# Kernel optimization log

Hardware: AMD Instinct MI355X
Metric: run time of the kernel (lower is better)

Reference implementation:

```python
import jax, jax.numpy as jnp
import numpy as np

N_STATE = 4      # d_state from CrossMambaFusionBlock(d_state=4)
DT_RANK = 48     # ceil(768/16), standard Mamba dt_rank='auto'
D_CONV = 4       # depthwise causal conv kernel size


def _ln(x, g, b):
    m = jnp.mean(x, axis=-1, keepdims=True)
    v = jnp.mean((x - m) ** 2, axis=-1, keepdims=True)
    return (x - m) * jax.lax.rsqrt(v + 1e-5) * g + b


def _dwconv1d(u, w, b):
    # u: (B,L,D); w: (D,1,K) depthwise causal conv along token dim L
    K = w.shape[-1]
    up = jnp.pad(jnp.transpose(u, (0, 2, 1)), ((0, 0), (0, 0), (K - 1, 0)))
    out = jax.lax.conv_general_dilated(up, w, (1,), 'VALID',
                                       feature_group_count=w.shape[0],
                                       dimension_numbers=('NCH', 'OIH', 'NCH'))
    return jnp.transpose(out, (0, 2, 1)) + b


def _pre(x, g, b, Win, Wconv, bconv, Wxp, Wdt, bdt):
    # LayerNorm -> in_proj -> depthwise conv + SiLU -> dt/B/C projections
    B_, H, W, C = x.shape
    xn = _ln(x, g, b).reshape(B_, H * W, C)
    u, z = jnp.split(xn @ Win, 2, axis=-1)              # (B,L,D) each
    u = jax.nn.silu(_dwconv1d(u, Wconv, bconv))
    dbl = u @ Wxp                                        # (B,L,R+2N)
    dtr, Bm, Cm = jnp.split(dbl, [DT_RANK, DT_RANK + N_STATE], axis=-1)
    dt = jax.nn.softplus(dtr @ Wdt + bdt)                # (B,L,D)
    return u, z, dt, Bm, Cm


def _selective_scan(u, dt, Alog, Bm, Cm, Dskip):
    # u, dt: (B,L,D); Alog: (D,N); Bm, Cm: (B,L,N)
    A = -jnp.exp(Alog)
    dA = jnp.exp(dt[..., None] * A)                      # (B,L,D,N) decay
    dBu = (dt * u)[..., None] * Bm[:, :, None, :]        # (B,L,D,N) input

    def comb(c1, c2):
        a1, h1 = c1
        a2, h2 = c2
        return a1 * a2, a2 * h1 + h2

    _, h = jax.lax.associative_scan(comb, (dA, dBu), axis=1)
    return jnp.einsum('bldn,bln->bld', h, Cm) + u * Dskip


def _forward(x1, x2,
             ln_g1, ln_b1, Win1, Wconv1, bconv1, Wxp1, Wdt1, bdt1, Alog1, Dskip1, Wout1,
             ln_g2, ln_b2, Win2, Wconv2, bconv2, Wxp2, Wdt2, bdt2, Alog2, Dskip2, Wout2):
    x1 = jnp.transpose(x1, (0, 2, 3, 1))  # BCHW -> BHWC (as in forward_features)
    x2 = jnp.transpose(x2, (0, 2, 3, 1))
    B_, H, W, C = x1.shape
    u1, z1, dt1, B1, C1 = _pre(x1, ln_g1, ln_b1, Win1, Wconv1, bconv1, Wxp1, Wdt1, bdt1)
    u2, z2, dt2, B2, C2 = _pre(x2, ln_g2, ln_b2, Win2, Wconv2, bconv2, Wxp2, Wdt2, bdt2)
    # Cross-modal fusion: each stream's SSM state is read out with the OTHER
    # stream's C projection (cross selective scan).
    y1 = _selective_scan(u1, dt1, Alog1, B1, C2, Dskip1)
    y2 = _selective_scan(u2, dt2, Alog2, B2, C1, Dskip2)
    o1 = ((y1 * jax.nn.silu(z1)) @ Wout1).reshape(B_, H, W, C)
    o2 = ((y2 * jax.nn.silu(z2)) @ Wout2).reshape(B_, H, W, C)
    return x1 + o1, x2 + o2


def setup_inputs():
    key = jax.random.key(0)
    ks = jax.random.split(key, 16)
    B_, C, H, W = 2, 768, 64, 64
    D = C  # d_inner (ssm_ratio = 1)

    def nrm(k, shape, s=0.02):
        return jax.random.normal(k, shape, jnp.float32) * s

    inp = {
        'x1': jax.random.normal(ks[0], (B_, C, H, W), jnp.float32),
        'x2': jax.random.normal(ks[1], (B_, C, H, W), jnp.float32),
    }
    for i, o in ((1, 2), (2, 8)):
        inp[f'ln_g{i}'] = jnp.ones((C,), jnp.float32)
        inp[f'ln_b{i}'] = jnp.zeros((C,), jnp.float32)
        inp[f'Win{i}'] = nrm(ks[o], (C, 2 * D))
        inp[f'Wconv{i}'] = nrm(ks[o + 1], (D, 1, D_CONV), 0.1)
        inp[f'bconv{i}'] = jnp.zeros((D,), jnp.float32)
        inp[f'Wxp{i}'] = nrm(ks[o + 2], (D, DT_RANK + 2 * N_STATE))
        inp[f'Wdt{i}'] = nrm(ks[o + 3], (DT_RANK, D), 0.05)
        inp[f'bdt{i}'] = jnp.full((D,), -4.6, jnp.float32)  # softplus -> dt ~ 0.01
        inp[f'Alog{i}'] = jnp.log(jnp.broadcast_to(
            jnp.arange(1, N_STATE + 1, dtype=jnp.float32), (D, N_STATE)))
        inp[f'Dskip{i}'] = jnp.ones((D,), jnp.float32)
        inp[f'Wout{i}'] = nrm(ks[o + 4], (D, C))
    return inp


def reference(x1, x2,
              ln_g1, ln_b1, Win1, Wconv1, bconv1, Wxp1, Wdt1, bdt1, Alog1, Dskip1, Wout1,
              ln_g2, ln_b2, Win2, Wconv2, bconv2, Wxp2, Wdt2, bdt2, Alog2, Dskip2, Wout2):
    return _forward(x1, x2,
                    ln_g1, ln_b1, Win1, Wconv1, bconv1, Wxp1, Wdt1, bdt1, Alog1, Dskip1, Wout1,
                    ln_g2, ln_b2, Win2, Wconv2, bconv2, Wxp2, Wdt2, bdt2, Alog2, Dskip2, Wout2)
```

## Files before the change

### kernel.cpp

```cpp
#include <hip/hip_runtime.h>
#include <cmath>

#define LDIM 4096
#define CDIM 768
#define BDIM 2
#define NST 4
#define RNK 48
#define CH 64
#define LC 64
#define NDT 896

typedef short bf16x8 __attribute__((ext_vector_type(8)));
typedef float f32x4 __attribute__((ext_vector_type(4)));

__device__ __forceinline__ float sigmoidf_(float x) { return 1.f / (1.f + __expf(-x)); }

__device__ __forceinline__ unsigned short f2bf(float f) {
    unsigned int u = __float_as_uint(f);
    u += 0x7fffu + ((u >> 16) & 1u);
    return (unsigned short)(u >> 16);
}
__device__ __forceinline__ float bf2f(unsigned short us) {
    unsigned int u = ((unsigned int)us) << 16;
    return __uint_as_float(u);
}

__device__ __forceinline__ void llds16(const unsigned short* g, unsigned short* l) {
    __builtin_amdgcn_global_load_lds(
        (const __attribute__((address_space(1))) unsigned int*)g,
        (__attribute__((address_space(3))) unsigned int*)l, 16, 0, 0);
}

__global__ __launch_bounds__(256) void stats_kernel(const float* __restrict__ x0,
                                                    const float* __restrict__ x1,
                                                    float* __restrict__ stats)
{
    int blk = blockIdx.x;
    int s = blk >> 7;
    int b = (blk >> 6) & 1;
    int l0 = (blk & 63) * 64;
    int wave = threadIdx.x >> 6, lane = threadIdx.x & 63;
    const float* x = s ? x1 : x0;
    const float* xp = x + ((size_t)b * CDIM) * LDIM + l0 + lane;
    float sm = 0.f, sq = 0.f;
    int cbeg = wave * 192;
#pragma unroll
    for (int i0 = 0; i0 < 192; i0 += 16) {
        float v[16];
#pragma unroll
        for (int j = 0; j < 16; j++) v[j] = xp[(size_t)(cbeg + i0 + j) * LDIM];
#pragma unroll
        for (int j = 0; j < 16; j++) { sm += v[j]; sq += v[j] * v[j]; }
    }
    __shared__ float red[2][4][64];
    red[0][wave][lane] = sm;
    red[1][wave][lane] = sq;
    __syncthreads();
    if (wave == 0) {
        float s_ = red[0][0][lane] + red[0][1][lane] + red[0][2][lane] + red[0][3][lane];
        float q_ = red[1][0][lane] + red[1][1][lane] + red[1][2][lane] + red[1][3][lane];
        float m = s_ * (1.f / CDIM);
        float var = q_ * (1.f / CDIM) - m * m;
        int idx = s * 8192 + b * LDIM + l0 + lane;
        stats[2 * idx] = m;
        stats[2 * idx + 1] = rsqrtf(var + 1e-5f);
    }
}

__global__ __launch_bounds__(256) void transpose_ln_kernel(
    const float* __restrict__ x0, const float* __restrict__ x1,
    const float* __restrict__ g0, const float* __restrict__ bb0,
    const float* __restrict__ g1, const float* __restrict__ bb1,
    const float* __restrict__ stats,
    unsigned short* __restrict__ xnb0, unsigned short* __restrict__ xnb1,
    float* __restrict__ out)
{
    __shared__ float tile[64][65];
    int t = threadIdx.x;
    int c0 = blockIdx.x * 64, l0 = blockIdx.y * 64;
    int z = blockIdx.z;
    int s = z >> 1, b = z & 1;
    const float* x = s ? x1 : x0;
    const float* g = s ? g1 : g0;
    const float* bb = s ? bb1 : bb0;
    unsigned short* xnb = s ? xnb1 : xnb0;
    int tl = t & 63, tg = t >> 6;
#pragma unroll
    for (int i = 0; i < 16; i++) {
        int cl = tg * 16 + i;
        tile[cl][tl] = x[((size_t)(b * CDIM + c0 + cl)) * LDIM + l0 + tl];
    }
    __syncthreads();
    const size_t SZ = (size_t)BDIM * LDIM * CDIM;
#pragma unroll
    for (int i = 0; i < 16; i++) {
        int ll = tg * 16 + i;
        int l = l0 + ll, c = c0 + tl;
        float v = tile[tl][ll];
        int sidx = s * 8192 + b * LDIM + l;
        float m = stats[sidx * 2], rs = stats[sidx * 2 + 1];
        size_t o = ((size_t)(b * LDIM + l)) * CDIM + c;
        out[(size_t)s * SZ + o] = v;
        xnb[o] = f2bf((v - m) * rs * g[c] + bb[c]);
    }
}

__global__ __launch_bounds__(256) void wt_transpose_all(
    const float* __restrict__ Win0, const float* __restrict__ Win1,
    const float* __restrict__ Wout0, const float* __restrict__ Wout1,
    unsigned short* __restrict__ WinT0, unsigned short* __restrict__ WinT1,
    unsigned short* __restrict__ WoutT0, unsigned short* __restrict__ WoutT1)
{
    int z = blockIdx.z;
    const float* W = (z == 0) ? Win0 : (z == 1) ? Win1 : (z == 2) ? Wout0 : Wout1;
    unsigned short* Wt = (z == 0) ? WinT0 : (z == 1) ? WinT1 : (z == 2) ? WoutT0 : WoutT1;
    const int K = CDIM;
    const int N = (z < 2) ? 2 * CDIM : CDIM;
    if (blockIdx.x * 64 >= N) return;
    __shared__ float tile[64][65];
    int t = threadIdx.x;
    int n0 = blockIdx.x * 64, k0 = blockIdx.y * 64;
    int tn = t & 63, tg = t >> 6;
#pragma unroll
    for (int i = 0; i < 16; i++) {
        int kl = tg * 16 + i;
        tile[kl][tn] = W[(size_t)(k0 + kl) * N + n0 + tn];
    }
    __syncthreads();
#pragma unroll
    for (int i = 0; i < 16; i++) {
        int nl = tg * 16 + i;
        int k = k0 + tn, n = n0 + nl;
        Wt[(size_t)n * K + k] = f2bf(tile[tn][nl]);
    }
}

__global__ __launch_bounds__(256) void wcomb_kernel(
    const float* __restrict__ Wxp0, const float* __restrict__ Wdt0,
    const float* __restrict__ Wxp1, const float* __restrict__ Wdt1,
    unsigned short* __restrict__ W0, unsigned short* __restrict__ W1)
{
    int s = blockIdx.z;
    const float* Wxp = s ? Wxp1 : Wxp0;
    const float* Wdt = s ? Wdt1 : Wdt0;
    unsigned short* WcombT = s ? W1 : W0;
    int t = threadIdx.x;
    int k = blockIdx.x * 64 + (t & 63);
    int n0 = blockIdx.y * 64;
    float wx[RNK];
#pragma unroll
    for (int r = 0; r < RNK; r++) wx[r] = Wxp[k * 56 + r];
    for (int i = (t >> 6); i < 64; i += 4) {
        int n = n0 + i;
        float val;
        if (n < CDIM) {
            float acc = 0.f;
#pragma unroll
            for (int r = 0; r < RNK; r++) acc += wx[r] * Wdt[(size_t)r * CDIM + n];
            val = acc;
        } else if (n < CDIM + 8) {
            val = Wxp[k * 56 + RNK + (n - CDIM)];
        } else {
            val = 0.f;
        }
        WcombT[(size_t)n * CDIM + k] = f2bf(val);
    }
}

__global__ __launch_bounds__(512, 4) void gemm_mfma(
    const unsigned short* __restrict__ A0, const unsigned short* __restrict__ A1,
    const unsigned short* __restrict__ Bt0, const unsigned short* __restrict__ Bt1,
    void* __restrict__ C0, void* __restrict__ C1, int ldc, int K, int epi,
    const float* __restrict__ bias0, const float* __restrict__ bias1,
    float* __restrict__ D0, float* __restrict__ D1)
{
    const unsigned short* A = blockIdx.z ? A1 : A0;
    const unsigned short* Bt = blockIdx.z ? Bt1 : Bt0;
    void* C = blockIdx.z ? C1 : C0;
    const float* bias = blockIdx.z ? bias1 : bias0;
    float* D = blockIdx.z ? D1 : D0;

    __shared__ unsigned short As[3][128 * 32];
    __shared__ unsigned short Bs[3][128 * 32];
    const int tid = threadIdx.x;
    const int wave = tid >> 6, lane = tid & 63;
    const int row0 = blockIdx.x * 128, col0 = blockIdx.y * 128;
    const int wm = (wave >> 2) * 64, wn = (wave & 3) * 32;
    f32x4 acc[4][2] = {};
    const int lr = lane >> 2;
    const int gi = ((lane & 3) ^ ((lane >> 3) & 3)) * 8;
    const int fr = lane & 15, fc = lane >> 4;

    const unsigned short* ga0 = A + (size_t)(row0 + wave * 16 + lr) * K + gi;
    const unsigned short* gb0 = Bt + (size_t)(col0 + wave * 16 + lr) * K + gi;
    const int rb = wave * 16;

#define ISSUE(st, kb)                         \
    do {                                      \
        llds16(ga0 + (kb), &As[st][rb * 32]); \
        llds16(gb0 + (kb), &Bs[st][rb * 32]); \
    } while (0)

    const int NIT = K / 32;
    ISSUE(0, 0);
    ISSUE(1, 32);
    for (int i = 0; i < NIT; i++) {
        if (i < NIT - 1) __builtin_amdgcn_s_waitcnt(0xF72);
        else __builtin_amdgcn_s_waitcnt(0xF70);
        __builtin_amdgcn_s_barrier();
        if (i + 2 < NIT) ISSUE((i + 2) % 3, (i + 2) * 32);
        const unsigned short* as = As[i % 3];
        const unsigned short* bs = Bs[i % 3];
        bf16x8 af[4], bfr[2];
#pragma unroll
        for (int ii = 0; ii < 4; ii++) {
            int r = wm + ii * 16 + fr;
            af[ii] = *(const bf16x8*)&as[r * 32 + (fc ^ ((r >> 1) & 3)) * 8];
        }
#pragma unroll
        for (int j = 0; j < 2; j++) {
            int r = wn + j * 16 + fr;
            bfr[j] = *(const bf16x8*)&bs[r * 32 + (fc ^ ((r >> 1) & 3)) * 8];
        }
#pragma unroll
        for (int ii = 0; ii < 4; ii++)
#pragma unroll
            for (int j = 0; j < 2; j++)
                acc[ii][j] = __builtin_amdgcn_mfma_f32_16x16x32_bf16(af[ii], bfr[j], acc[ii][j], 0, 0, 0);
    }
#undef ISSUE

    const int cr = (lane >> 4) * 4, cc = lane & 15;
#pragma unroll
    for (int ii = 0; ii < 4; ii++)
#pragma unroll
        for (int j = 0; j < 2; j++) {
            int col = col0 + wn + j * 16 + cc;
#pragma unroll
            for (int r = 0; r < 4; r++) {
                int row = row0 + wm + ii * 16 + cr + r;
                float v = acc[ii][j][r];
                if (epi == 1) {
                    float* Cf = (float*)C;
                    size_t o = (size_t)row * ldc + col;
                    Cf[o] = v + Cf[o];
                } else if (epi == 2) {
                    if (col < CDIM) {
                        v += bias[col];
                        v = (v > 20.f) ? v : __logf(1.f + __expf(v));
                        ((unsigned short*)C)[(size_t)row * ldc + col] = f2bf(v);
                    } else if (col < CDIM + 8) {
                        D[(size_t)row * 8 + (col - CDIM)] = v;
                    }
                } else {
                    ((unsigned short*)C)[(size_t)row * ldc + col] = f2bf(v);
                }
            }
        }
}

__global__ __launch_bounds__(256) void conv_silu_kernel(
    const unsigned short* __restrict__ uzb0, const unsigned short* __restrict__ uzb1,
    const float* __restrict__ w0, const float* __restrict__ bc0,
    const float* __restrict__ w1, const float* __restrict__ bc1,
    unsigned short* __restrict__ ub0, unsigned short* __restrict__ ub1)
{
    int s = blockIdx.y;
    const unsigned short* uzb = s ? uzb1 : uzb0;
    const float* w = s ? w1 : w0;
    const float* bc = s ? bc1 : bc0;
    unsigned short* ub = s ? ub1 : ub0;
    int idx = blockIdx.x * 256 + threadIdx.x;
    int d8 = (idx % 96) * 8;
    int bl = idx / 96;
    int l = bl & (LDIM - 1);

    float wr[8][4];
#pragma unroll
    for (int q = 0; q < 8; q++) {
        f32x4 wv = *(const f32x4*)&w[(d8 + q) * 4];
#pragma unroll
        for (int k = 0; k < 4; k++) wr[q][k] = wv[k];
    }
    float acc[8];
    f32x4 b0 = *(const f32x4*)&bc[d8];
    f32x4 b1 = *(const f32x4*)&bc[d8 + 4];
#pragma unroll
    for (int q = 0; q < 4; q++) { acc[q] = b0[q]; acc[4 + q] = b1[q]; }

#pragma unroll
    for (int k = 0; k < 4; k++) {
        int ls = l - 3 + k;
        if (ls >= 0) {
            bf16x8 uv = *(const bf16x8*)&uzb[(size_t)(bl - 3 + k) * (2 * CDIM) + d8];
#pragma unroll
            for (int q = 0; q < 8; q++)
                acc[q] += bf2f((unsigned short)uv[q]) * wr[q][k];
        }
    }
    bf16x8 ov;
#pragma unroll
    for (int q = 0; q < 8; q++) {
        float v = acc[q];
        ov[q] = (short)f2bf(v * sigmoidf_(v));
    }
    *(bf16x8*)&ub[(size_t)bl * CDIM + d8] = ov;
}

__global__ __launch_bounds__(256) void scan_phaseA(
    const unsigned short* __restrict__ u0, const unsigned short* __restrict__ dt0,
    const float* __restrict__ dbl0, const float* __restrict__ Alog0,
    const unsigned short* __restrict__ u1, const unsigned short* __restrict__ dt1,
    const float* __restrict__ dbl1, const float* __restrict__ Alog1,
    float* __restrict__ agg)
{
    int idx = blockIdx.x * 256 + threadIdx.x;
    int d = idx % CDIM;
    int t1 = idx / CDIM;
    int c = t1 % CH;
    int t2 = t1 / CH;
    int b = t2 & 1;
    int s = t2 >> 1;
    const unsigned short* u = s ? u1 : u0;
    const unsigned short* dt = s ? dt1 : dt0;
    const float* dbl = s ? dbl1 : dbl0;
    const float* Alog = s ? Alog1 : Alog0;
    float A[4];
#pragma unroll
    for (int n = 0; n < 4; n++) A[n] = -__expf(Alog[d * 4 + n]);
    float h[4] = {0, 0, 0, 0}, aa[4] = {1, 1, 1, 1};
    int rowb = b * LDIM + c * LC;
    for (int t = 0; t < LC; t++) {
        int row = rowb + t;
        float dtv = bf2f(dt[(size_t)row * CDIM + d]);
        float uv = bf2f(u[(size_t)row * CDIM + d]);
        float du = dtv * uv;
        const float* bm = dbl + (size_t)row * 8;
#pragma unroll
        for (int n = 0; n < 4; n++) {
            float dA = __expf(dtv * A[n]);
            h[n] = dA * h[n] + du * bm[n];
            aa[n] *= dA;
        }
    }
    float* o = agg + (size_t)idx * 8;
#pragma unroll
    for (int n = 0; n < 4; n++) { o[n] = aa[n]; o[4 + n] = h[n]; }
}

__global__ __launch_bounds__(256) void scan_phaseB(const float* __restrict__ agg,
                                                   float* __restrict__ hinit)
{
    int idx = blockIdx.x * 256 + threadIdx.x;
    int d = idx % CDIM;
    int sb = idx / CDIM;
    float st[4] = {0, 0, 0, 0};
    for (int c = 0; c < CH; c++) {
        size_t base = ((size_t)sb * CH + c) * CDIM + d;
        const float* a = agg + base * 8;
        float* hi = hinit + base * 4;
#pragma unroll
        for (int n = 0; n < 4; n++) hi[n] = st[n];
#pragma unroll
        for (int n = 0; n < 4; n++) st[n] = a[n] * st[n] + a[4 + n];
    }
}

__global__ __launch_bounds__(256) void scan_phaseC(
    const unsigned short* __restrict__ u0, const unsigned short* __restrict__ dt0,
    const unsigned short* __restrict__ uzb0, const float* __restrict__ dbl0,
    const float* __restrict__ Alog0, const float* __restrict__ Dsk0, unsigned short* __restrict__ g0,
    const unsigned short* __restrict__ u1, const unsigned short* __restrict__ dt1,
    const unsigned short* __restrict__ uzb1, const float* __restrict__ dbl1,
    const float* __restrict__ Alog1, const float* __restrict__ Dsk1, unsigned short* __restrict__ g1,
    const float* __restrict__ hinit)
{
    int idx = blockIdx.x * 256 + threadIdx.x;
    int d = idx % CDIM;
    int t1 = idx / CDIM;
    int c = t1 % CH;
    int t2 = t1 / CH;
    int b = t2 & 1;
    int s = t2 >> 1;
    const unsigned short* u = s ? u1 : u0;
    const unsigned short* dt = s ? dt1 : dt0;
    const unsigned short* uzb = s ? uzb1 : uzb0;
    const float* dbl = s ? dbl1 : dbl0;
    const float* dblO = s ? dbl0 : dbl1;
    const float* Alog = s ? Alog1 : Alog0;
    const float* Dsk = s ? Dsk1 : Dsk0;
    unsigned short* gated = s ? g1 : g0;
    float A[4];
#pragma unroll
    for (int n = 0; n < 4; n++) A[n] = -__expf(Alog[d * 4 + n]);
    float Dv = Dsk[d];
    float h[4];
    const float* hi = hinit + (size_t)idx * 4;
#pragma unroll
    for (int n = 0; n < 4; n++) h[n] = hi[n];
    int rowb = b * LDIM + c * LC;
    for (int t = 0; t < LC; t++) {
        int row = rowb + t;
        float dtv = bf2f(dt[(size_t)row * CDIM + d]);
        float uv = bf2f(u[(size_t)row * CDIM + d]);
        float du = dtv * uv;
        const float* bm = dbl + (size_t)row * 8;
        const float* cm = dblO + (size_t)row * 8 + 4;
        float y = 0.f;
#pragma unroll
        for (int n = 0; n < 4; n++) {
            float dA = __expf(dtv * A[n]);
            h[n] = dA * h[n] + du * bm[n];
            y += h[n] * cm[n];
        }
        y += uv * Dv;
        float zv = bf2f(uzb[(size_t)row * (2 * CDIM) + CDIM + d]);
        gated[(size_t)row * CDIM + d] = f2bf(y * (zv * sigmoidf_(zv)));
    }
}

extern "C" void kernel_launch(void* const* d_in, const int* in_sizes, int n_in,
                              void* d_out, int out_size, void* d_ws, size_t ws_size,
                              hipStream_t stream)
{
    const float* x[2] = {(const float*)d_in[0], (const float*)d_in[1]};
    const float *ln_g[2], *ln_b[2], *Win[2], *Wconv[2], *bconv[2], *Wxp[2],
        *Wdt[2], *bdt[2], *Alog[2], *Dskip[2], *Wout[2];
    for (int s = 0; s < 2; s++) {
        int base = 2 + s * 11;
        ln_g[s] = (const float*)d_in[base + 0];
        ln_b[s] = (const float*)d_in[base + 1];
        Win[s] = (const float*)d_in[base + 2];
        Wconv[s] = (const float*)d_in[base + 3];
        bconv[s] = (const float*)d_in[base + 4];
        Wxp[s] = (const float*)d_in[base + 5];
        Wdt[s] = (const float*)d_in[base + 6];
        bdt[s] = (const float*)d_in[base + 7];
        Alog[s] = (const float*)d_in[base + 8];
        Dskip[s] = (const float*)d_in[base + 9];
        Wout[s] = (const float*)d_in[base + 10];
    }

    const int M = BDIM * LDIM;
    char* base = (char*)d_ws;
    auto alloc = [&](size_t bytes) {
        char* p = base;
        base += (bytes + 255) & ~(size_t)255;
        return p;
    };
    unsigned short* uzb[2] = {(unsigned short*)alloc((size_t)M * 1536 * 2),
                              (unsigned short*)alloc((size_t)M * 1536 * 2)};
    unsigned short* dtb[2] = {(unsigned short*)alloc((size_t)M * CDIM * 2),
                              (unsigned short*)alloc((size_t)M * CDIM * 2)};
    unsigned short* ub[2] = {(unsigned short*)alloc((size_t)M * CDIM * 2),
                             (unsigned short*)alloc((size_t)M * CDIM * 2)};
    unsigned short* xnb[2] = {(unsigned short*)alloc((size_t)M * CDIM * 2),
                              (unsigned short*)alloc((size_t)M * CDIM * 2)};
    float* dbl[2] = {(float*)alloc((size_t)M * 8 * 4), (float*)alloc((size_t)M * 8 * 4)};
    unsigned short* WinT[2] = {(unsigned short*)alloc(1536 * 768 * 2),
                               (unsigned short*)alloc(1536 * 768 * 2)};
    unsigned short* WoutT[2] = {(unsigned short*)alloc(768 * 768 * 2),
                                (unsigned short*)alloc(768 * 768 * 2)};
    unsigned short* WcombT[2] = {(unsigned short*)alloc((size_t)NDT * 768 * 2),
                                 (unsigned short*)alloc((size_t)NDT * 768 * 2)};
    float* agg = (float*)alloc((size_t)2 * BDIM * CH * CDIM * 8 * 4);
    float* hinit = (float*)alloc((size_t)2 * BDIM * CH * CDIM * 4 * 4);
    float* stats = (float*)alloc((size_t)2 * M * 2 * 4);

    dim3 blk(256);
    dim3 blk512(512);
    const size_t SZ = (size_t)BDIM * LDIM * CDIM;

    stats_kernel<<<dim3(256), blk, 0, stream>>>(x[0], x[1], stats);
    transpose_ln_kernel<<<dim3(CDIM / 64, LDIM / 64, 4), blk, 0, stream>>>(
        x[0], x[1], ln_g[0], ln_b[0], ln_g[1], ln_b[1], stats, xnb[0], xnb[1], (float*)d_out);

    wt_transpose_all<<<dim3(1536 / 64, 768 / 64, 4), blk, 0, stream>>>(
        Win[0], Win[1], Wout[0], Wout[1], WinT[0], WinT[1], WoutT[0], WoutT[1]);
    wcomb_kernel<<<dim3(768 / 64, NDT / 64, 2), blk, 0, stream>>>(
        Wxp[0], Wdt[0], Wxp[1], Wdt[1], WcombT[0], WcombT[1]);

    gemm_mfma<<<dim3(M / 128, 1536 / 128, 2), blk512, 0, stream>>>(
        xnb[0], xnb[1], WinT[0], WinT[1], uzb[0], uzb[1], 2 * CDIM, CDIM, 3,
        nullptr, nullptr, nullptr, nullptr);

    conv_silu_kernel<<<dim3((M * CDIM / 8) / 256, 2), blk, 0, stream>>>(
        uzb[0], uzb[1], Wconv[0], bconv[0], Wconv[1], bconv[1], ub[0], ub[1]);

    gemm_mfma<<<dim3(M / 128, NDT / 128, 2), blk512, 0, stream>>>(
        ub[0], ub[1], WcombT[0], WcombT[1], dtb[0], dtb[1], CDIM, CDIM, 2,
        bdt[0], bdt[1], dbl[0], dbl[1]);

    scan_phaseA<<<dim3((2 * BDIM * CH * CDIM) / 256), blk, 0, stream>>>(
        ub[0], dtb[0], dbl[0], Alog[0], ub[1], dtb[1], dbl[1], Alog[1], agg);
    scan_phaseB<<<dim3((2 * BDIM * CDIM) / 256), blk, 0, stream>>>(agg, hinit);
    scan_phaseC<<<dim3((2 * BDIM * CH * CDIM) / 256), blk, 0, stream>>>(
        ub[0], dtb[0], uzb[0], dbl[0], Alog[0], Dskip[0], xnb[0],
        ub[1], dtb[1], uzb[1], dbl[1], Alog[1], Dskip[1], xnb[1], hinit);

    float* out = (float*)d_out;
    gemm_mfma<<<dim3(M / 128, CDIM / 128, 2), blk512, 0, stream>>>(
        xnb[0], xnb[1], WoutT[0], WoutT[1], out, out + SZ, CDIM, CDIM, 1,
        nullptr, nullptr, nullptr, nullptr);
}
```

Measured before the change: 435.0 us.

## Enlarge GEMM tiles to 256xN with 64-deep K double buffering and setprio

Rewrites the bf16 MFMA GEMM to use 256-row by 192- or 256-column block tiles with 64-wide K stages. It double-buffers the stages instead of triple-buffering 32-wide ones and interleaves fragment loads with MFMA batches using barriers and s_setprio. The goal is more data reuse per LDS load and fewer loop iterations and barriers per FLOP. NDT is padded from 896 to 1024 so the dt projection fits 256-wide tiles, which adds wasted compute on zero columns. The larger tiles also mean far fewer blocks per GPU and lower occupancy (launch bounds 2 instead of 4).

```diff
diff --git a/kernel.cpp b/kernel.cpp
--- a/kernel.cpp
+++ b/kernel.cpp
@@ -8,7 +8,7 @@
 #define RNK 48
 #define CH 64
 #define LC 64
-#define NDT 896
+#define NDT 1024
 
 typedef short bf16x8 __attribute__((ext_vector_type(8)));
 typedef float f32x4 __attribute__((ext_vector_type(4)));
@@ -167,7 +167,8 @@
     }
 }
 
-__global__ __launch_bounds__(512, 4) void gemm_mfma(
+template <int NW>
+__global__ __launch_bounds__(512, 2) void gemm_mfma(
     const unsigned short* __restrict__ A0, const unsigned short* __restrict__ A1,
     const unsigned short* __restrict__ Bt0, const unsigned short* __restrict__ Bt1,
     void* __restrict__ C0, void* __restrict__ C1, int ldc, int K, int epi,
@@ -180,66 +181,117 @@
     const float* bias = blockIdx.z ? bias1 : bias0;
     float* D = blockIdx.z ? D1 : D0;
 
-    __shared__ unsigned short As[3][128 * 32];
-    __shared__ unsigned short Bs[3][128 * 32];
+    constexpr int BN = NW * 64;
+    __shared__ unsigned short As[2][256 * 64];
+    __shared__ unsigned short Bs[2][BN * 64];
+
     const int tid = threadIdx.x;
     const int wave = tid >> 6, lane = tid & 63;
-    const int row0 = blockIdx.x * 128, col0 = blockIdx.y * 128;
-    const int wm = (wave >> 2) * 64, wn = (wave & 3) * 32;
-    f32x4 acc[4][2] = {};
-    const int lr = lane >> 2;
-    const int gi = ((lane & 3) ^ ((lane >> 3) & 3)) * 8;
+    const int row0 = blockIdx.x * 256, col0 = blockIdx.y * BN;
+    const int wm = (wave >> 2) * 128;
+    const int wn = (wave & 3) * (NW * 16);
+    f32x4 acc[8][NW] = {};
+
+    const int rs = tid >> 3;
+    const int kcg = (tid & 7) ^ (rs & 7);
+    const unsigned short* gA = A + (size_t)(row0 + rs) * K + kcg * 8;
+    const unsigned short* gB = Bt + (size_t)(col0 + rs) * K + kcg * 8;
+    const size_t rK = (size_t)64 * K;
     const int fr = lane & 15, fc = lane >> 4;
 
-    const unsigned short* ga0 = A + (size_t)(row0 + wave * 16 + lr) * K + gi;
-    const unsigned short* gb0 = Bt + (size_t)(col0 + wave * 16 + lr) * K + gi;
-    const int rb = wave * 16;
-
-#define ISSUE(st, kb)                         \
-    do {                                      \
-        llds16(ga0 + (kb), &As[st][rb * 32]); \
-        llds16(gb0 + (kb), &Bs[st][rb * 32]); \
+    auto ldfrag = [&](const unsigned short* s, int row, int kc) -> bf16x8 {
+        return *(const bf16x8*)&s[row * 64 + ((kc ^ (row & 7)) << 3)];
+    };
+
+#define GSTAGE(nb, kt)                                                  \
+    do {                                                                \
+        const unsigned short* a_ = gA + (size_t)(kt) * 64;              \
+        const unsigned short* b_ = gB + (size_t)(kt) * 64;              \
+        unsigned short* al = &As[nb][wave * 512];                       \
+        unsigned short* bl = &Bs[nb][wave * 512];                       \
+        _Pragma("unroll")                                               \
+        for (int r_ = 0; r_ < 4; r_++) llds16(a_ + r_ * rK, al + r_ * 4096); \
+        _Pragma("unroll")                                               \
+        for (int r_ = 0; r_ < NW; r_++) llds16(b_ + r_ * rK, bl + r_ * 4096); \
     } while (0)
 
-    const int NIT = K / 32;
-    ISSUE(0, 0);
-    ISSUE(1, 32);
-    for (int i = 0; i < NIT; i++) {
-        if (i < NIT - 1) __builtin_amdgcn_s_waitcnt(0xF72);
-        else __builtin_amdgcn_s_waitcnt(0xF70);
-        __builtin_amdgcn_s_barrier();
-        if (i + 2 < NIT) ISSUE((i + 2) % 3, (i + 2) * 32);
-        const unsigned short* as = As[i % 3];
-        const unsigned short* bs = Bs[i % 3];
-        bf16x8 af[4], bfr[2];
-#pragma unroll
-        for (int ii = 0; ii < 4; ii++) {
-            int r = wm + ii * 16 + fr;
-            af[ii] = *(const bf16x8*)&as[r * 32 + (fc ^ ((r >> 1) & 3)) * 8];
-        }
-#pragma unroll
-        for (int j = 0; j < 2; j++) {
-            int r = wn + j * 16 + fr;
-            bfr[j] = *(const bf16x8*)&bs[r * 32 + (fc ^ ((r >> 1) & 3)) * 8];
-        }
-#pragma unroll
-        for (int ii = 0; ii < 4; ii++)
-#pragma unroll
-            for (int j = 0; j < 2; j++)
-                acc[ii][j] = __builtin_amdgcn_mfma_f32_16x16x32_bf16(af[ii], bfr[j], acc[ii][j], 0, 0, 0);
-    }
-#undef ISSUE
+    const int NKT = K / 64;
+    GSTAGE(0, 0);
+    __builtin_amdgcn_s_waitcnt(0xF70);
+    __builtin_amdgcn_s_barrier();
+
+    for (int kt = 0; kt < NKT; kt++) {
+        const int cur = kt & 1;
+        const unsigned short* as = As[cur];
+        const unsigned short* bs = Bs[cur];
+        bf16x8 af[4], bfv[NW];
+
+        if (kt + 1 < NKT) GSTAGE(cur ^ 1, kt + 1);
+#pragma unroll
+        for (int mi = 0; mi < 4; mi++) af[mi] = ldfrag(as, wm + mi * 16 + fr, fc);
+#pragma unroll
+        for (int nj = 0; nj < NW; nj++) bfv[nj] = ldfrag(bs, wn + nj * 16 + fr, fc);
+        __builtin_amdgcn_s_barrier();
+        __builtin_amdgcn_s_setprio(1);
+#pragma unroll
+        for (int mi = 0; mi < 4; mi++)
+#pragma unroll
+            for (int nj = 0; nj < NW; nj++)
+                acc[mi][nj] = __builtin_amdgcn_mfma_f32_16x16x32_bf16(af[mi], bfv[nj], acc[mi][nj], 0, 0, 0);
+        __builtin_amdgcn_s_setprio(0);
+        __builtin_amdgcn_s_barrier();
+
+#pragma unroll
+        for (int mi = 0; mi < 4; mi++) af[mi] = ldfrag(as, wm + 64 + mi * 16 + fr, fc);
+        __builtin_amdgcn_s_barrier();
+        __builtin_amdgcn_s_setprio(1);
+#pragma unroll
+        for (int mi = 0; mi < 4; mi++)
+#pragma unroll
+            for (int nj = 0; nj < NW; nj++)
+                acc[4 + mi][nj] = __builtin_amdgcn_mfma_f32_16x16x32_bf16(af[mi], bfv[nj], acc[4 + mi][nj], 0, 0, 0);
+        __builtin_amdgcn_s_setprio(0);
+        __builtin_amdgcn_s_barrier();
+
+#pragma unroll
+        for (int mi = 0; mi < 4; mi++) af[mi] = ldfrag(as, wm + mi * 16 + fr, 4 + fc);
+#pragma unroll
+        for (int nj = 0; nj < NW; nj++) bfv[nj] = ldfrag(bs, wn + nj * 16 + fr, 4 + fc);
+        __builtin_amdgcn_s_barrier();
+        __builtin_amdgcn_s_setprio(1);
+#pragma unroll
+        for (int mi = 0; mi < 4; mi++)
+#pragma unroll
+            for (int nj = 0; nj < NW; nj++)
+                acc[mi][nj] = __builtin_amdgcn_mfma_f32_16x16x32_bf16(af[mi], bfv[nj], acc[mi][nj], 0, 0, 0);
+        __builtin_amdgcn_s_setprio(0);
+        __builtin_amdgcn_s_barrier();
+
+#pragma unroll
+        for (int mi = 0; mi < 4; mi++) af[mi] = ldfrag(as, wm + 64 + mi * 16 + fr, 4 + fc);
+        __builtin_amdgcn_s_barrier();
+        __builtin_amdgcn_s_setprio(1);
+#pragma unroll
+        for (int mi = 0; mi < 4; mi++)
+#pragma unroll
+            for (int nj = 0; nj < NW; nj++)
+                acc[4 + mi][nj] = __builtin_amdgcn_mfma_f32_16x16x32_bf16(af[mi], bfv[nj], acc[4 + mi][nj], 0, 0, 0);
+        __builtin_amdgcn_s_setprio(0);
+        if (kt + 1 < NKT) __builtin_amdgcn_s_waitcnt(0xF70);
+        __builtin_amdgcn_s_barrier();
+    }
+#undef GSTAGE
 
     const int cr = (lane >> 4) * 4, cc = lane & 15;
 #pragma unroll
-    for (int ii = 0; ii < 4; ii++)
-#pragma unroll
-        for (int j = 0; j < 2; j++) {
-            int col = col0 + wn + j * 16 + cc;
+    for (int mi = 0; mi < 8; mi++)
+#pragma unroll
+        for (int nj = 0; nj < NW; nj++) {
+            int col = col0 + wn + nj * 16 + cc;
 #pragma unroll
             for (int r = 0; r < 4; r++) {
-                int row = row0 + wm + ii * 16 + cr + r;
-                float v = acc[ii][j][r];
+                int row = row0 + wm + mi * 16 + cr + r;
+                float v = acc[mi][nj][r];
                 if (epi == 1) {
                     float* Cf = (float*)C;
                     size_t o = (size_t)row * ldc + col;
@@ -480,14 +532,14 @@
     wcomb_kernel<<<dim3(768 / 64, NDT / 64, 2), blk, 0, stream>>>(
         Wxp[0], Wdt[0], Wxp[1], Wdt[1], WcombT[0], WcombT[1]);
 
-    gemm_mfma<<<dim3(M / 128, 1536 / 128, 2), blk512, 0, stream>>>(
+    gemm_mfma<3><<<dim3(M / 256, 1536 / 192, 2), blk512, 0, stream>>>(
         xnb[0], xnb[1], WinT[0], WinT[1], uzb[0], uzb[1], 2 * CDIM, CDIM, 3,
         nullptr, nullptr, nullptr, nullptr);
 
     conv_silu_kernel<<<dim3((M * CDIM / 8) / 256, 2), blk, 0, stream>>>(
         uzb[0], uzb[1], Wconv[0], bconv[0], Wconv[1], bconv[1], ub[0], ub[1]);
 
-    gemm_mfma<<<dim3(M / 128, NDT / 128, 2), blk512, 0, stream>>>(
+    gemm_mfma<4><<<dim3(M / 256, NDT / 256, 2), blk512, 0, stream>>>(
         ub[0], ub[1], WcombT[0], WcombT[1], dtb[0], dtb[1], CDIM, CDIM, 2,
         bdt[0], bdt[1], dbl[0], dbl[1]);
 
@@ -499,7 +551,7 @@
         ub[1], dtb[1], uzb[1], dbl[1], Alog[1], Dskip[1], xnb[1], hinit);
 
     float* out = (float*)d_out;
-    gemm_mfma<<<dim3(M / 128, CDIM / 128, 2), blk512, 0, stream>>>(
+    gemm_mfma<3><<<dim3(M / 256, CDIM / 192, 2), blk512, 0, stream>>>(
         xnb[0], xnb[1], WoutT[0], WoutT[1], out, out + SZ, CDIM, CDIM, 1,
         nullptr, nullptr, nullptr, nullptr);
 }
```

After: 490.1 us. 12.7% more time.
